# Optimization experiments

Hardware: AMD Instinct MI355X
Metric: run time of the kernel (lower is better)

Reference implementation:

```python
import jax, jax.numpy as jnp
import numpy as np

# Involution-style aggregation (SAN Aggregation, pad_mode=0 / zero padding)
K, STRIDE, PAD, DIL = 3, 1, 1, 1


def setup_inputs() -> dict:
    key = jax.random.key(0)
    k1, k2 = jax.random.split(key)
    B, C, H, W = 8, 256, 64, 64
    WC = 16  # weight channels (channel groups share a kernel)
    OH = (H + 2 * PAD - (DIL * (K - 1) + 1)) // STRIDE + 1
    OW = (W + 2 * PAD - (DIL * (K - 1) + 1)) // STRIDE + 1
    x = jax.random.normal(k1, (B, C, H, W), dtype=jnp.float32)
    weight = jax.random.normal(k2, (B, WC, K * K, OH * OW), dtype=jnp.float32)
    return {"x": x, "weight": weight}


def reference(x, weight):
    B, C, H, W = x.shape
    _, WC, K2, _ = weight.shape
    OH = (H + 2 * PAD - (DIL * (K - 1) + 1)) // STRIDE + 1
    OW = (W + 2 * PAD - (DIL * (K - 1) + 1)) // STRIDE + 1
    G = C // WC  # channel groups sharing each dynamic kernel
    xp = jnp.pad(x, ((0, 0), (0, 0), (PAD, PAD), (PAD, PAD)))  # zero pad
    # weight per tap: [B, 1, WC, OH, OW] broadcast over groups
    w = weight.reshape(B, 1, WC, K2, OH, OW)
    out = jnp.zeros((B, G, WC, OH, OW), dtype=x.dtype)
    # fixed small K^2 loop over kernel taps; accumulate without materializing
    # the full unfolded [B, C, K^2, OH, OW] tensor
    for idx in range(K2):
        i, j = idx // K, idx % K
        xs = xp[:, :, i * DIL:i * DIL + (OH - 1) * STRIDE + 1:STRIDE,
                      j * DIL:j * DIL + (OW - 1) * STRIDE + 1:STRIDE]
        out = out + xs.reshape(B, G, WC, OH, OW) * w[:, :, :, idx]
    return out.reshape(B, C, OH, OW)
```

## Files before the change

### kernel.cpp

```cpp
#include <hip/hip_runtime.h>


#define NB 8
#define NC 256
#define NH 64
#define NW 64
#define NWC 16
#define NG 16
#define STRIP 8
#define LCHR 10
#define LROW 64
#define LCH (LCHR * LROW)

__global__ __launch_bounds__(256, 4) void agg_kernel(const float* __restrict__ x,
                                                     const float* __restrict__ wt,
                                                     float* __restrict__ out) {
    __shared__ float lds[NG * LCH];

    const int tid   = threadIdx.x;
    const int l16   = tid & 15;
    const int row   = (tid >> 4) & 7;
    const int h     = tid >> 7;
    const int bid   = blockIdx.x;
    const int strip = bid & 7;
    const int wc    = (bid >> 3) & 15;
    const int b     = bid >> 7;

    const int oh  = strip * STRIP + row;
    const int ow0 = l16 * 4;
    const int r0  = strip * STRIP - 1;

    float4 sv[10];
    int    laddr[10];
#pragma unroll
    for (int k = 0; k < 10; ++k) {
        const int f   = tid + k * 256;
        const int ch  = f / 160;
        const int rem = f - ch * 160;
        const int r   = rem >> 4;
        const int c4  = rem & 15;
        const int gr  = r0 + r;
        float4 v = make_float4(0.f, 0.f, 0.f, 0.f);
        if ((unsigned)gr < (unsigned)NH) {
            const int c = ch * NWC + wc;
            v = *reinterpret_cast<const float4*>(
                x + (((b * NC + c) * NH + gr) * NW) + c4 * 4);
        }
        sv[k]    = v;
        laddr[k] = ch * LCH + r * LROW + c4 * 4;
    }

    float w[9][4];
    {
        const float* wp = wt + ((b * NWC + wc) * 9) * (NH * NW) + oh * NW + ow0;
#pragma unroll
        for (int idx = 0; idx < 9; ++idx) {
            float4 t = *reinterpret_cast<const float4*>(wp + idx * (NH * NW));
            w[idx][0] = t.x; w[idx][1] = t.y; w[idx][2] = t.z; w[idx][3] = t.w;
        }
    }

#pragma unroll
    for (int k = 0; k < 10; ++k) {
        *reinterpret_cast<float4*>(&lds[laddr[k]]) = sv[k];
    }

    __syncthreads();

    const bool has_left  = (l16 > 0);
    const bool has_right = (l16 < 15);

#pragma unroll
    for (int cc = 0; cc < 8; ++cc) {
        const int ch = h * 8 + cc;
        const float* pch = &lds[ch * LCH];
        float acc[4] = {0.f, 0.f, 0.f, 0.f};

#pragma unroll
        for (int i = 0; i < 3; ++i) {
            const float* p = pch + (row + i) * LROW + ow0;
            float4 m = *reinterpret_cast<const float4*>(p);
            const float e0 = has_left  ? p[-1] : 0.f;
            const float e5 = has_right ? p[4]  : 0.f;
            const float e[6] = {e0, m.x, m.y, m.z, m.w, e5};
#pragma unroll
            for (int j = 0; j < 3; ++j) {
                const float* wj = w[i * 3 + j];
                acc[0] += e[0 + j] * wj[0];
                acc[1] += e[1 + j] * wj[1];
                acc[2] += e[2 + j] * wj[2];
                acc[3] += e[3 + j] * wj[3];
            }
        }

        float* op = out + (((b * NC + ch * NWC + wc) * NH + oh) * NW) + ow0;
        *reinterpret_cast<float4*>(op) = make_float4(acc[0], acc[1], acc[2], acc[3]);
    }
}

extern "C" void kernel_launch(void* const* d_in, const int* in_sizes, int n_in,
                              void* d_out, int out_size, void* d_ws, size_t ws_size,
                              hipStream_t stream) {
    const float* x  = (const float*)d_in[0];
    const float* wt = (const float*)d_in[1];
    float* out      = (float*)d_out;

    dim3 grid(NB * NWC * 8);
    dim3 block(256);
    agg_kernel<<<grid, block, 0, stream>>>(x, wt, out);
}
```

Before: 21.39 us.

## Split LDS staging into two halves, overlap loads with compute, use DPP halos

The channel staging into LDS is split into two halves: the second half's global loads are issued after the first barrier and overlap with computing the first half's channels. Horizontal halo values now come from DPP row shifts of neighbouring lanes, with bound_ctrl zero filling at the 16-lane row edges, instead of extra scalar LDS reads. Block indices are remapped so consecutive hardware blocks spread across batches and strips. This aims to hide global load latency and cut LDS traffic, at the cost of a second barrier and more live registers.

```diff
diff --git a/kernel.cpp b/kernel.cpp
--- a/kernel.cpp
+++ b/kernel.cpp
@@ -11,6 +11,16 @@
 #define LCHR 10
 #define LROW 64
 #define LCH (LCHR * LROW)
+#define HCH 8
+
+__device__ __forceinline__ float dpp_shr1(float v) {
+    return __int_as_float(__builtin_amdgcn_update_dpp(
+        0, __float_as_int(v), 0x111, 0xf, 0xf, true));
+}
+__device__ __forceinline__ float dpp_shl1(float v) {
+    return __int_as_float(__builtin_amdgcn_update_dpp(
+        0, __float_as_int(v), 0x101, 0xf, 0xf, true));
+}
 
 __global__ __launch_bounds__(256, 4) void agg_kernel(const float* __restrict__ x,
                                                      const float* __restrict__ wt,
@@ -20,8 +30,10 @@
     const int tid   = threadIdx.x;
     const int l16   = tid & 15;
     const int row   = (tid >> 4) & 7;
-    const int h     = tid >> 7;
-    const int bid   = blockIdx.x;
+    const int c4sel = tid >> 7;
+
+    const int hw    = blockIdx.x;
+    const int bid   = (hw & 7) * 128 + (hw >> 3);
     const int strip = bid & 7;
     const int wc    = (bid >> 3) & 15;
     const int b     = bid >> 7;
@@ -30,25 +42,25 @@
     const int ow0 = l16 * 4;
     const int r0  = strip * STRIP - 1;
 
-    float4 sv[10];
-    int    laddr[10];
-#pragma unroll
-    for (int k = 0; k < 10; ++k) {
+    auto stage_issue = [&](int k, int half, float4& v, int& addr) {
         const int f   = tid + k * 256;
         const int ch  = f / 160;
         const int rem = f - ch * 160;
         const int r   = rem >> 4;
         const int c4  = rem & 15;
         const int gr  = r0 + r;
-        float4 v = make_float4(0.f, 0.f, 0.f, 0.f);
+        v = make_float4(0.f, 0.f, 0.f, 0.f);
         if ((unsigned)gr < (unsigned)NH) {
-            const int c = ch * NWC + wc;
+            const int c = (half * HCH + ch) * NWC + wc;
             v = *reinterpret_cast<const float4*>(
                 x + (((b * NC + c) * NH + gr) * NW) + c4 * 4);
         }
-        sv[k]    = v;
-        laddr[k] = ch * LCH + r * LROW + c4 * 4;
-    }
+        addr = (half * HCH + ch) * LCH + r * LROW + c4 * 4;
+    };
+
+    float4 s0[5]; int a0[5];
+#pragma unroll
+    for (int k = 0; k < 5; ++k) stage_issue(k, 0, s0[k], a0[k]);
 
     float w[9][4];
     {
@@ -61,41 +73,49 @@
     }
 
 #pragma unroll
-    for (int k = 0; k < 10; ++k) {
-        *reinterpret_cast<float4*>(&lds[laddr[k]]) = sv[k];
-    }
+    for (int k = 0; k < 5; ++k) *reinterpret_cast<float4*>(&lds[a0[k]]) = s0[k];
+
+    auto compute_half = [&](int half) {
+#pragma unroll
+        for (int cc = 0; cc < 4; ++cc) {
+            const int g = half * HCH + c4sel * 4 + cc;
+            const float* pch = &lds[g * LCH];
+            float acc[4] = {0.f, 0.f, 0.f, 0.f};
+#pragma unroll
+            for (int i = 0; i < 3; ++i) {
+                const float* p = pch + (row + i) * LROW + ow0;
+                float4 m = *reinterpret_cast<const float4*>(p);
+                const float e0 = dpp_shr1(m.w);
+                const float e5 = dpp_shl1(m.x);
+                const float e[6] = {e0, m.x, m.y, m.z, m.w, e5};
+#pragma unroll
+                for (int j = 0; j < 3; ++j) {
+                    const float* wj = w[i * 3 + j];
+                    acc[0] += e[0 + j] * wj[0];
+                    acc[1] += e[1 + j] * wj[1];
+                    acc[2] += e[2 + j] * wj[2];
+                    acc[3] += e[3 + j] * wj[3];
+                }
+            }
+            float* op = out + (((b * NC + g * NWC + wc) * NH + oh) * NW) + ow0;
+            *reinterpret_cast<float4*>(op) = make_float4(acc[0], acc[1], acc[2], acc[3]);
+        }
+    };
 
     __syncthreads();
 
-    const bool has_left  = (l16 > 0);
-    const bool has_right = (l16 < 15);
+    float4 s1[5]; int a1[5];
+#pragma unroll
+    for (int k = 0; k < 5; ++k) stage_issue(k, 1, s1[k], a1[k]);
+
+    compute_half(0);
 
 #pragma unroll
-    for (int cc = 0; cc < 8; ++cc) {
-        const int ch = h * 8 + cc;
-        const float* pch = &lds[ch * LCH];
-        float acc[4] = {0.f, 0.f, 0.f, 0.f};
+    for (int k = 0; k < 5; ++k) *reinterpret_cast<float4*>(&lds[a1[k]]) = s1[k];
 
-#pragma unroll
-        for (int i = 0; i < 3; ++i) {
-            const float* p = pch + (row + i) * LROW + ow0;
-            float4 m = *reinterpret_cast<const float4*>(p);
-            const float e0 = has_left  ? p[-1] : 0.f;
-            const float e5 = has_right ? p[4]  : 0.f;
-            const float e[6] = {e0, m.x, m.y, m.z, m.w, e5};
-#pragma unroll
-            for (int j = 0; j < 3; ++j) {
-                const float* wj = w[i * 3 + j];
-                acc[0] += e[0 + j] * wj[0];
-                acc[1] += e[1 + j] * wj[1];
-                acc[2] += e[2 + j] * wj[2];
-                acc[3] += e[3 + j] * wj[3];
-            }
-        }
+    __syncthreads();
 
-        float* op = out + (((b * NC + ch * NWC + wc) * NH + oh) * NW) + ow0;
-        *reinterpret_cast<float4*>(op) = make_float4(acc[0], acc[1], acc[2], acc[3]);
-    }
+    compute_half(1);
 }
 
 extern "C" void kernel_launch(void* const* d_in, const int* in_sizes, int n_in,
```

New measurement: 21.54 us. About the same (+0.7%).

## Enlarge row strips, use DPP lane shifts for halos, nontemporal stores, XCD-aware block mapping

Applied to the files above, without the earlier changes.

Each block now covers a 16-row strip over all 16 channel groups, where it used to cover an 8-row strip split across two thread halves. The halo overhead drops from 10/8 to 18/16 rows loaded. The left and right neighbour values now come from DPP row shifts within each 16-lane row (bound_ctrl gives zero at the edges) instead of extra LDS reads. Output stores are nontemporal, and block IDs are remapped so neighbouring work lands on the same XCD. The trade-off is double the LDS (72KB per block) and half the grid, which lowers occupancy to 2 blocks per CU.

```diff
diff --git a/kernel.cpp b/kernel.cpp
--- a/kernel.cpp
+++ b/kernel.cpp
@@ -7,36 +7,48 @@
 #define NW 64
 #define NWC 16
 #define NG 16
-#define STRIP 8
-#define LCHR 10
+#define STRIP 16
+#define LCHR 18
 #define LROW 64
 #define LCH (LCHR * LROW)
 
-__global__ __launch_bounds__(256, 4) void agg_kernel(const float* __restrict__ x,
+typedef float f32x4 __attribute__((ext_vector_type(4)));
+
+__device__ __forceinline__ float dpp_shr1(float v) {
+    return __int_as_float(__builtin_amdgcn_update_dpp(
+        0, __float_as_int(v), 0x111, 0xf, 0xf, true));
+}
+__device__ __forceinline__ float dpp_shl1(float v) {
+    return __int_as_float(__builtin_amdgcn_update_dpp(
+        0, __float_as_int(v), 0x101, 0xf, 0xf, true));
+}
+
+__global__ __launch_bounds__(256, 2) void agg_kernel(const float* __restrict__ x,
                                                      const float* __restrict__ wt,
                                                      float* __restrict__ out) {
     __shared__ float lds[NG * LCH];
 
-    const int tid   = threadIdx.x;
-    const int l16   = tid & 15;
-    const int row   = (tid >> 4) & 7;
-    const int h     = tid >> 7;
-    const int bid   = blockIdx.x;
-    const int strip = bid & 7;
-    const int wc    = (bid >> 3) & 15;
-    const int b     = bid >> 7;
+    const int tid = threadIdx.x;
+    const int l16 = tid & 15;
+    const int row = tid >> 4;
 
-    const int oh  = strip * STRIP + row;
+    const int hw   = blockIdx.x;
+    const int bid  = (hw & 7) * 64 + (hw >> 3);
+    const int q    = bid & 3;
+    const int wc   = (bid >> 2) & 15;
+    const int b    = bid >> 6;
+
+    const int oh  = q * STRIP + row;
     const int ow0 = l16 * 4;
-    const int r0  = strip * STRIP - 1;
+    const int r0  = q * STRIP - 1;
 
-    float4 sv[10];
-    int    laddr[10];
+    float4 sv[18];
+    int    laddr[18];
 #pragma unroll
-    for (int k = 0; k < 10; ++k) {
+    for (int k = 0; k < 18; ++k) {
         const int f   = tid + k * 256;
-        const int ch  = f / 160;
-        const int rem = f - ch * 160;
+        const int ch  = f / 288;
+        const int rem = f - ch * 288;
         const int r   = rem >> 4;
         const int c4  = rem & 15;
         const int gr  = r0 + r;
@@ -61,18 +73,14 @@
     }
 
 #pragma unroll
-    for (int k = 0; k < 10; ++k) {
+    for (int k = 0; k < 18; ++k) {
         *reinterpret_cast<float4*>(&lds[laddr[k]]) = sv[k];
     }
 
     __syncthreads();
 
-    const bool has_left  = (l16 > 0);
-    const bool has_right = (l16 < 15);
-
 #pragma unroll
-    for (int cc = 0; cc < 8; ++cc) {
-        const int ch = h * 8 + cc;
+    for (int ch = 0; ch < NG; ++ch) {
         const float* pch = &lds[ch * LCH];
         float acc[4] = {0.f, 0.f, 0.f, 0.f};
 
@@ -80,8 +88,8 @@
         for (int i = 0; i < 3; ++i) {
             const float* p = pch + (row + i) * LROW + ow0;
             float4 m = *reinterpret_cast<const float4*>(p);
-            const float e0 = has_left  ? p[-1] : 0.f;
-            const float e5 = has_right ? p[4]  : 0.f;
+            const float e0 = dpp_shr1(m.w);
+            const float e5 = dpp_shl1(m.x);
             const float e[6] = {e0, m.x, m.y, m.z, m.w, e5};
 #pragma unroll
             for (int j = 0; j < 3; ++j) {
@@ -94,7 +102,8 @@
         }
 
         float* op = out + (((b * NC + ch * NWC + wc) * NH + oh) * NW) + ow0;
-        *reinterpret_cast<float4*>(op) = make_float4(acc[0], acc[1], acc[2], acc[3]);
+        f32x4 o = {acc[0], acc[1], acc[2], acc[3]};
+        __builtin_nontemporal_store(o, reinterpret_cast<f32x4*>(op));
     }
 }
 
@@ -105,7 +114,7 @@
     const float* wt = (const float*)d_in[1];
     float* out      = (float*)d_out;
 
-    dim3 grid(NB * NWC * 8);
+    dim3 grid(NB * NWC * 4);
     dim3 block(256);
     agg_kernel<<<grid, block, 0, stream>>>(x, wt, out);
 }
```

Result: faster. 20.83 us (-2.6%).
